# Kernel optimization log

Hardware: AMD Instinct MI355X
Metric: run time of the kernel (lower is better)

The kernel has to match this reference:

```python
import jax, jax.numpy as jnp
import numpy as np

B, S, D, E, F = 2, 1024, 1024, 14, 2048

def setup_inputs() -> dict:
    key = jax.random.key(0)
    k0, k1, k2, k3 = jax.random.split(key, 4)
    h = jax.random.normal(k0, (B, S, D), jnp.float32)
    gate_w = jax.random.normal(k1, (E, D), jnp.float32) * 0.02
    # kaiming-uniform-ish scale for expert weights
    w1 = jax.random.normal(k2, (E, D, F), jnp.float32) * (1.0 / np.sqrt(D).astype(np.float32))
    b1 = jnp.zeros((E, F), jnp.float32)
    w2 = jax.random.normal(k3, (E, F, D), jnp.float32) * (1.0 / np.sqrt(F).astype(np.float32))
    b2 = jnp.zeros((E, D), jnp.float32)
    return {"h": h, "gate_w": gate_w, "w1": w1, "b1": b1, "w2": w2, "b2": b2}

def reference(h, gate_w, w1, b1, w2, b2):
    # Eval-mode forward (no expert dropout, router_step=None, return_aux=False path)
    Bb, Ss, Dd = h.shape
    x = h.reshape(Bb * Ss, Dd)                       # (N, D)
    logits = x @ gate_w.T                            # (N, E)
    probs = jax.nn.softmax(logits, axis=-1)
    top2_p, top2_i = jax.lax.top_k(probs, 2)         # (N, 2)
    w = top2_p / jnp.maximum(top2_p.sum(-1, keepdims=True), 1e-10)
    # dense all-experts FFN
    hh = jnp.einsum('nd,edf->nef', x, w1) + b1       # (N, E, F)
    hh = jax.nn.gelu(hh, approximate=False)          # torch F.gelu default = exact erf
    all_out = jnp.einsum('nef,efd->ned', hh, w2) + b2  # (N, E, D)
    n = jnp.arange(x.shape[0])
    out0 = all_out[n, top2_i[:, 0]]                  # (N, D)
    out1 = all_out[n, top2_i[:, 1]]
    moe_out = w[:, 0:1] * out0 + w[:, 1:2] * out1
    result = jnp.clip(x + moe_out, -100.0, 100.0).reshape(Bb, Ss, Dd)
    return result
```

## Files before the change

kernel.cpp:

```cpp
#include <hip/hip_runtime.h>
#include <cstdint>
#include <cstddef>

#define NTOK 2048
#define DDIM 1024
#define FDIM 2048
#define NEXP 14
#define MAXT 2048

typedef __attribute__((ext_vector_type(8))) short short8;
typedef __attribute__((ext_vector_type(4))) float floatx4;

__device__ __forceinline__ unsigned pack2bf(float lo, float hi) {
    unsigned a = __float_as_uint(lo), b = __float_as_uint(hi);
    return ((a + 0x8000u) >> 16) | ((b + 0x8000u) & 0xffff0000u);
}
__device__ __forceinline__ unsigned short f2bf1(float f) {
    return (unsigned short)((__float_as_uint(f) + 0x8000u) >> 16);
}

__device__ __forceinline__ void glds16(const void* g, void* lds) {
    __builtin_amdgcn_global_load_lds((const __attribute__((address_space(1))) unsigned*)g,
                                     (__attribute__((address_space(3))) unsigned*)lds, 16, 0, 0);
}

__global__ __launch_bounds__(256) void cvtx_kernel(const float* __restrict__ x,
                                                   unsigned short* __restrict__ xb,
                                                   int* __restrict__ cnt) {
    if (blockIdx.x == 0 && threadIdx.x < NEXP) cnt[threadIdx.x] = 0;
    const size_t i = ((size_t)blockIdx.x * 256 + threadIdx.x) * 8;
    float4 a = *(const float4*)(x + i);
    float4 b = *(const float4*)(x + i + 4);
    uint4 u;
    u.x = pack2bf(a.x, a.y); u.y = pack2bf(a.z, a.w);
    u.z = pack2bf(b.x, b.y); u.w = pack2bf(b.z, b.w);
    *(uint4*)(xb + i) = u;
}

__global__ __launch_bounds__(256) void gate_kernel(
    const float* __restrict__ x, const float* __restrict__ gw,
    int* __restrict__ cnt, int* __restrict__ lists, float* __restrict__ wt)
{
    const int wave = threadIdx.x >> 6, lane = threadIdx.x & 63;
    const int n = blockIdx.x * 4 + wave;
    float part[NEXP];
#pragma unroll
    for (int e = 0; e < NEXP; ++e) part[e] = 0.f;
    const float4* xr = (const float4*)(x + (size_t)n * DDIM);
#pragma unroll
    for (int kk = 0; kk < 4; ++kk) {
        const float4 xv = xr[kk * 64 + lane];
#pragma unroll
        for (int e = 0; e < NEXP; ++e) {
            const float4 g = ((const float4*)(gw + e * DDIM))[kk * 64 + lane];
            part[e] = fmaf(xv.x, g.x, fmaf(xv.y, g.y, fmaf(xv.z, g.z, fmaf(xv.w, g.w, part[e]))));
        }
    }
#pragma unroll
    for (int e = 0; e < NEXP; ++e) {
        float v = part[e];
        for (int off = 32; off; off >>= 1) v += __shfl_xor(v, off);
        part[e] = v;
    }
    int i0 = 0; float l0 = part[0];
#pragma unroll
    for (int e = 1; e < NEXP; ++e) if (part[e] > l0) { l0 = part[e]; i0 = e; }
    int i1 = -1; float l1 = -3.0e38f;
#pragma unroll
    for (int e = 0; e < NEXP; ++e) if (e != i0 && part[e] > l1) { l1 = part[e]; i1 = e; }
    if (lane == 0) {
        const float r  = __expf(l1 - l0);
        wt[2 * n]     = 1.f / (1.f + r);
        wt[2 * n + 1] = r / (1.f + r);
        int p0 = atomicAdd(&cnt[i0], 1); lists[i0 * MAXT + p0] = 2 * n;
        int p1 = atomicAdd(&cnt[i1], 1); lists[i1 * MAXT + p1] = 2 * n + 1;
    }
}

#define MAXJOBS 78
__global__ void jobs_kernel(const int* __restrict__ cnt, int* __restrict__ job_e,
                            int* __restrict__ job_mt, int* __restrict__ njobs) {
    if (threadIdx.x == 0) {
        int J = 0;
        for (int e = 0; e < NEXP; ++e) {
            const int m = (cnt[e] + 63) >> 6;
            for (int i = 0; i < m; ++i) { job_e[J] = e; job_mt[J] = i; ++J; }
        }
        njobs[0] = J;
    }
}

__global__ __launch_bounds__(256) void gemm1_kernel(
    const unsigned short* __restrict__ xb, const float* __restrict__ w1,
    const float* __restrict__ b1, const int* __restrict__ cnt,
    const int* __restrict__ lists, const int* __restrict__ job_e,
    const int* __restrict__ job_mt, const int* __restrict__ njobs,
    unsigned short* __restrict__ hh)
{
    const int j = blockIdx.y;
    if (j >= njobs[0]) return;
    const int e = job_e[j], mt = job_mt[j], nt = blockIdx.x;
    const int count = cnt[e];
    const int* list = lists + e * MAXT + mt * 64;
    const int mloc = min(64, count - mt * 64);

    __shared__ __align__(16) unsigned short As[2][64 * 32];
    __shared__ __align__(16) unsigned short Bs[2][128 * 32];

    const int t = threadIdx.x, lane = t & 63, wave = t >> 6;
    const int lrow = lane & 15, lq = lane >> 4;
    const int wn = wave * 32;

    const int arow = wave * 16 + (lane >> 2);
    const int atok = list[min(arow, mloc - 1)] >> 1;
    const unsigned short* aG = xb + (size_t)atok * DDIM + (lane & 3) * 8;
    const int bn = t & 127, bg = t >> 7;
    const float* bG = w1 + (size_t)e * DDIM * FDIM + nt * 128 + bn;

    floatx4 acc[4][2];
#pragma unroll
    for (int i = 0; i < 4; ++i)
#pragma unroll
        for (int jn = 0; jn < 2; ++jn) acc[i][jn] = (floatx4)0.f;

    float br[2][8];
    glds16(aG, &As[0][wave * 512]);
#pragma unroll
    for (int c = 0; c < 2; ++c) {
        const int kc = bg + 2 * c;
#pragma unroll
        for (int jj = 0; jj < 8; ++jj) br[c][jj] = bG[(size_t)(kc * 8 + jj) * FDIM];
    }
#pragma unroll
    for (int c = 0; c < 2; ++c) {
        const int kc = bg + 2 * c;
        uint4 u;
        u.x = pack2bf(br[c][0], br[c][1]); u.y = pack2bf(br[c][2], br[c][3]);
        u.z = pack2bf(br[c][4], br[c][5]); u.w = pack2bf(br[c][6], br[c][7]);
        *(uint4*)&Bs[0][bn * 32 + ((kc ^ (bn & 3)) * 8)] = u;
    }
#pragma unroll
    for (int c = 0; c < 2; ++c) {
        const int kc = bg + 2 * c;
#pragma unroll
        for (int jj = 0; jj < 8; ++jj) br[c][jj] = bG[(size_t)(32 + kc * 8 + jj) * FDIM];
    }

    int p = 0;
    for (int k0 = 0; k0 < DDIM; k0 += 32) {
        __syncthreads();
        if (k0 + 32 < DDIM) {
            glds16(aG + k0 + 32, &As[p ^ 1][wave * 512]);
#pragma unroll
            for (int c = 0; c < 2; ++c) {
                const int kc = bg + 2 * c;
                uint4 u;
                u.x = pack2bf(br[c][0], br[c][1]); u.y = pack2bf(br[c][2], br[c][3]);
                u.z = pack2bf(br[c][4], br[c][5]); u.w = pack2bf(br[c][6], br[c][7]);
                *(uint4*)&Bs[p ^ 1][bn * 32 + ((kc ^ (bn & 3)) * 8)] = u;
            }
        }
        if (k0 + 64 < DDIM) {
#pragma unroll
            for (int c = 0; c < 2; ++c) {
                const int kc = bg + 2 * c;
#pragma unroll
                for (int jj = 0; jj < 8; ++jj) br[c][jj] = bG[(size_t)(k0 + 64 + kc * 8 + jj) * FDIM];
            }
        }
        short8 af[4], bf[2];
#pragma unroll
        for (int i = 0; i < 4; ++i)
            af[i] = *(const short8*)&As[p][(i * 16 + lrow) * 32 + lq * 8];
#pragma unroll
        for (int jn = 0; jn < 2; ++jn) {
            const int n = wn + jn * 16 + lrow;
            bf[jn] = *(const short8*)&Bs[p][n * 32 + ((lq ^ (n & 3)) * 8)];
        }
#pragma unroll
        for (int i = 0; i < 4; ++i)
#pragma unroll
            for (int jn = 0; jn < 2; ++jn)
                acc[i][jn] = __builtin_amdgcn_mfma_f32_16x16x32_bf16(af[i], bf[jn], acc[i][jn], 0, 0, 0);
        p ^= 1;
    }
#pragma unroll
    for (int jn = 0; jn < 2; ++jn) {
        const int n = nt * 128 + wn + jn * 16 + lrow;
        const float bias = b1[e * FDIM + n];
#pragma unroll
        for (int i = 0; i < 4; ++i) {
#pragma unroll
            for (int r = 0; r < 4; ++r) {
                const int m = i * 16 + lq * 4 + r;
                if (m < mloc) {
                    const int pp = list[m];
                    float v = acc[i][jn][r] + bias;
                    v = 0.5f * v * (1.0f + erff(v * 0.70710678118654752f));
                    hh[(size_t)pp * FDIM + n] = f2bf1(v);
                }
            }
        }
    }
}

__global__ __launch_bounds__(256) void gemm2_kernel(
    const unsigned short* __restrict__ hh, const float* __restrict__ w2,
    const float* __restrict__ b2, const int* __restrict__ cnt,
    const int* __restrict__ lists, const int* __restrict__ job_e,
    const int* __restrict__ job_mt, const int* __restrict__ njobs,
    const float* __restrict__ wt, float* __restrict__ out0, float* __restrict__ out1)
{
    const int j = blockIdx.y;
    if (j >= njobs[0]) return;
    const int e = job_e[j], mt = job_mt[j], nt = blockIdx.x;
    const int count = cnt[e];
    const int* list = lists + e * MAXT + mt * 64;
    const int mloc = min(64, count - mt * 64);

    __shared__ __align__(16) unsigned short As[2][64 * 32];
    __shared__ __align__(16) unsigned short Bs[2][64 * 32];

    const int t = threadIdx.x, lane = t & 63, wave = t >> 6;
    const int lrow = lane & 15, lq = lane >> 4;
    const int wm = (wave & 1) * 32, wn = (wave >> 1) * 16;

    const int arow = wave * 16 + (lane >> 2);
    const int apair = list[min(arow, mloc - 1)];
    const unsigned short* aG = hh + (size_t)apair * FDIM + (lane & 3) * 8;
    const int bn = t & 63, bkc = t >> 6;
    const float* bG = w2 + (size_t)e * FDIM * DDIM + nt * 64 + bn;

    floatx4 acc[2][2];
#pragma unroll
    for (int i = 0; i < 2; ++i)
#pragma unroll
        for (int jn = 0; jn < 2; ++jn) acc[i][jn] = (floatx4)0.f;

    float br[8];
    glds16(aG, &As[0][wave * 512]);
#pragma unroll
    for (int jj = 0; jj < 8; ++jj) br[jj] = bG[(size_t)(bkc * 8 + jj) * DDIM];
    {
        uint4 u;
        u.x = pack2bf(br[0], br[1]); u.y = pack2bf(br[2], br[3]);
        u.z = pack2bf(br[4], br[5]); u.w = pack2bf(br[6], br[7]);
        *(uint4*)&Bs[0][bn * 32 + ((bkc ^ (bn & 3)) * 8)] = u;
    }
#pragma unroll
    for (int jj = 0; jj < 8; ++jj) br[jj] = bG[(size_t)(32 + bkc * 8 + jj) * DDIM];

    int p = 0;
    for (int k0 = 0; k0 < FDIM; k0 += 32) {
        __syncthreads();
        if (k0 + 32 < FDIM) {
            glds16(aG + k0 + 32, &As[p ^ 1][wave * 512]);
            uint4 u;
            u.x = pack2bf(br[0], br[1]); u.y = pack2bf(br[2], br[3]);
            u.z = pack2bf(br[4], br[5]); u.w = pack2bf(br[6], br[7]);
            *(uint4*)&Bs[p ^ 1][bn * 32 + ((bkc ^ (bn & 3)) * 8)] = u;
        }
        if (k0 + 64 < FDIM) {
#pragma unroll
            for (int jj = 0; jj < 8; ++jj) br[jj] = bG[(size_t)(k0 + 64 + bkc * 8 + jj) * DDIM];
        }
        short8 af[2], bf[2];
#pragma unroll
        for (int i = 0; i < 2; ++i)
            af[i] = *(const short8*)&As[p][(wm + i * 16 + lrow) * 32 + lq * 8];
#pragma unroll
        for (int jn = 0; jn < 2; ++jn) {
            const int n = wn + jn * 16 + lrow;
            bf[jn] = *(const short8*)&Bs[p][((wn * 2) + jn * 16 + lrow) * 32 + ((lq ^ (((wn * 2) + jn * 16 + lrow) & 3)) * 8)];
        }
#pragma unroll
        for (int i = 0; i < 2; ++i)
#pragma unroll
            for (int jn = 0; jn < 2; ++jn)
                acc[i][jn] = __builtin_amdgcn_mfma_f32_16x16x32_bf16(af[i], bf[jn], acc[i][jn], 0, 0, 0);
        p ^= 1;
    }
#pragma unroll
    for (int jn = 0; jn < 2; ++jn) {
        const int n = nt * 64 + (wn * 2) + jn * 16 + lrow;
        const float bias = b2[e * DDIM + n];
#pragma unroll
        for (int i = 0; i < 2; ++i) {
#pragma unroll
            for (int r = 0; r < 4; ++r) {
                const int m = wm + i * 16 + lq * 4 + r;
                if (m < mloc) {
                    const int pp = list[m];
                    const int tok = pp >> 1;
                    const float v = (acc[i][jn][r] + bias) * wt[pp];
                    float* dst = (pp & 1) ? out1 : out0;
                    dst[(size_t)tok * DDIM + n] = v;
                }
            }
        }
    }
}

__global__ __launch_bounds__(256) void finalize_kernel(
    const float* __restrict__ x, const float* __restrict__ o1,
    float* __restrict__ out)
{
    const size_t i = ((size_t)blockIdx.x * 256 + threadIdx.x) * 4;
    float4 xv = *(const float4*)(x + i);
    float4 a  = *(const float4*)(out + i);
    float4 b  = *(const float4*)(o1 + i);
    float4 r;
    r.x = fminf(fmaxf(xv.x + a.x + b.x, -100.f), 100.f);
    r.y = fminf(fmaxf(xv.y + a.y + b.y, -100.f), 100.f);
    r.z = fminf(fmaxf(xv.z + a.z + b.z, -100.f), 100.f);
    r.w = fminf(fmaxf(xv.w + a.w + b.w, -100.f), 100.f);
    *(float4*)(out + i) = r;
}

extern "C" void kernel_launch(void* const* d_in, const int* in_sizes, int n_in,
                              void* d_out, int out_size, void* d_ws, size_t ws_size,
                              hipStream_t stream) {
    const float* h  = (const float*)d_in[0];
    const float* gw = (const float*)d_in[1];
    const float* w1 = (const float*)d_in[2];
    const float* b1 = (const float*)d_in[3];
    const float* w2 = (const float*)d_in[4];
    const float* b2 = (const float*)d_in[5];
    float* out = (float*)d_out;

    char* ws = (char*)d_ws;
    int*   cnt    = (int*)ws;
    int*   lists  = (int*)(ws + 256);
    float* wt     = (float*)(ws + 114944);
    int*   job_e  = (int*)(ws + 131328);
    int*   job_mt = (int*)(ws + 131840);
    int*   njobs  = (int*)(ws + 132352);
    unsigned short* xb = (unsigned short*)(ws + 262144);
    float* o1     = (float*)(ws + 262144 + 4194304);
    unsigned short* hhb = (unsigned short*)(ws + 262144 + 4194304 + 8388608);

    cvtx_kernel<<<NTOK * DDIM / (256 * 8), 256, 0, stream>>>(h, xb, cnt);
    gate_kernel<<<NTOK / 4, 256, 0, stream>>>(h, gw, cnt, lists, wt);
    jobs_kernel<<<1, 64, 0, stream>>>(cnt, job_e, job_mt, njobs);
    gemm1_kernel<<<dim3(FDIM / 128, MAXJOBS), 256, 0, stream>>>(xb, w1, b1, cnt, lists, job_e, job_mt, njobs, hhb);
    gemm2_kernel<<<dim3(DDIM / 64, MAXJOBS), 256, 0, stream>>>(hhb, w2, b2, cnt, lists, job_e, job_mt, njobs, wt, out, o1);
    finalize_kernel<<<NTOK * DDIM / (256 * 4), 256, 0, stream>>>(h, o1, out);
}
```

Measured before the change: 433.7 us.

## Pre-convert expert weights to transposed bf16 and stream via direct LDS loads

Result: slower. 541.9 us (+25.0%).

```diff
diff --git a/kernel.cpp b/kernel.cpp
--- a/kernel.cpp
+++ b/kernel.cpp
@@ -37,6 +37,28 @@
     *(uint4*)(xb + i) = u;
 }
 
+__global__ __launch_bounds__(256) void cvtw_kernel(
+    const float* __restrict__ src, unsigned short* __restrict__ dst,
+    int K, int N, int kt, int tpe)
+{
+    const int b = blockIdx.x;
+    const int e = b / tpe, r = b % tpe;
+    const int n = (r / kt) * 64 + (threadIdx.x & 63);
+    const int kq = (r % kt) * 128 + (threadIdx.x >> 6) * 32;
+    const float* s = src + (size_t)e * K * N + (size_t)kq * N + n;
+    float v[32];
+#pragma unroll
+    for (int j = 0; j < 32; ++j) v[j] = s[(size_t)j * N];
+    unsigned us[16];
+#pragma unroll
+    for (int q = 0; q < 16; ++q) us[q] = pack2bf(v[2 * q], v[2 * q + 1]);
+    unsigned short* d = dst + (size_t)e * K * N + (size_t)n * K + kq;
+    *(uint4*)(d)      = uint4{us[0],  us[1],  us[2],  us[3]};
+    *(uint4*)(d + 8)  = uint4{us[4],  us[5],  us[6],  us[7]};
+    *(uint4*)(d + 16) = uint4{us[8],  us[9],  us[10], us[11]};
+    *(uint4*)(d + 24) = uint4{us[12], us[13], us[14], us[15]};
+}
+
 __global__ __launch_bounds__(256) void gate_kernel(
     const float* __restrict__ x, const float* __restrict__ gw,
     int* __restrict__ cnt, int* __restrict__ lists, float* __restrict__ wt)
@@ -91,7 +113,7 @@
 }
 
 __global__ __launch_bounds__(256) void gemm1_kernel(
-    const unsigned short* __restrict__ xb, const float* __restrict__ w1,
+    const unsigned short* __restrict__ xb, const unsigned short* __restrict__ w1t,
     const float* __restrict__ b1, const int* __restrict__ cnt,
     const int* __restrict__ lists, const int* __restrict__ job_e,
     const int* __restrict__ job_mt, const int* __restrict__ njobs,
@@ -107,15 +129,15 @@
     __shared__ __align__(16) unsigned short As[2][64 * 32];
     __shared__ __align__(16) unsigned short Bs[2][128 * 32];
 
-    const int t = threadIdx.x, lane = t & 63, wave = t >> 6;
+    const int t = threadIdx.x, lane = t & 63, w = t >> 6;
     const int lrow = lane & 15, lq = lane >> 4;
-    const int wn = wave * 32;
-
-    const int arow = wave * 16 + (lane >> 2);
+
+    const int arow = w * 16 + lrow;
     const int atok = list[min(arow, mloc - 1)] >> 1;
-    const unsigned short* aG = xb + (size_t)atok * DDIM + (lane & 3) * 8;
-    const int bn = t & 127, bg = t >> 7;
-    const float* bG = w1 + (size_t)e * DDIM * FDIM + nt * 128 + bn;
+    const unsigned short* aG = xb + (size_t)atok * DDIM + lq * 8;
+    const int nA = nt * 128 + w * 16 + lrow;
+    const unsigned short* bG0 = w1t + ((size_t)e * FDIM + nA) * DDIM + lq * 8;
+    const unsigned short* bG1 = bG0 + (size_t)64 * DDIM;
 
     floatx4 acc[4][2];
 #pragma unroll
@@ -123,60 +145,25 @@
 #pragma unroll
         for (int jn = 0; jn < 2; ++jn) acc[i][jn] = (floatx4)0.f;
 
-    float br[2][8];
-    glds16(aG, &As[0][wave * 512]);
-#pragma unroll
-    for (int c = 0; c < 2; ++c) {
-        const int kc = bg + 2 * c;
-#pragma unroll
-        for (int jj = 0; jj < 8; ++jj) br[c][jj] = bG[(size_t)(kc * 8 + jj) * FDIM];
-    }
-#pragma unroll
-    for (int c = 0; c < 2; ++c) {
-        const int kc = bg + 2 * c;
-        uint4 u;
-        u.x = pack2bf(br[c][0], br[c][1]); u.y = pack2bf(br[c][2], br[c][3]);
-        u.z = pack2bf(br[c][4], br[c][5]); u.w = pack2bf(br[c][6], br[c][7]);
-        *(uint4*)&Bs[0][bn * 32 + ((kc ^ (bn & 3)) * 8)] = u;
-    }
-#pragma unroll
-    for (int c = 0; c < 2; ++c) {
-        const int kc = bg + 2 * c;
-#pragma unroll
-        for (int jj = 0; jj < 8; ++jj) br[c][jj] = bG[(size_t)(32 + kc * 8 + jj) * FDIM];
-    }
+    glds16(aG, &As[0][w * 512]);
+    glds16(bG0, &Bs[0][w * 512]);
+    glds16(bG1, &Bs[0][(w + 4) * 512]);
 
     int p = 0;
     for (int k0 = 0; k0 < DDIM; k0 += 32) {
         __syncthreads();
         if (k0 + 32 < DDIM) {
-            glds16(aG + k0 + 32, &As[p ^ 1][wave * 512]);
-#pragma unroll
-            for (int c = 0; c < 2; ++c) {
-                const int kc = bg + 2 * c;
-                uint4 u;
-                u.x = pack2bf(br[c][0], br[c][1]); u.y = pack2bf(br[c][2], br[c][3]);
-                u.z = pack2bf(br[c][4], br[c][5]); u.w = pack2bf(br[c][6], br[c][7]);
-                *(uint4*)&Bs[p ^ 1][bn * 32 + ((kc ^ (bn & 3)) * 8)] = u;
-            }
-        }
-        if (k0 + 64 < DDIM) {
-#pragma unroll
-            for (int c = 0; c < 2; ++c) {
-                const int kc = bg + 2 * c;
-#pragma unroll
-                for (int jj = 0; jj < 8; ++jj) br[c][jj] = bG[(size_t)(k0 + 64 + kc * 8 + jj) * FDIM];
-            }
+            glds16(aG + k0 + 32, &As[p ^ 1][w * 512]);
+            glds16(bG0 + k0 + 32, &Bs[p ^ 1][w * 512]);
+            glds16(bG1 + k0 + 32, &Bs[p ^ 1][(w + 4) * 512]);
         }
         short8 af[4], bf[2];
 #pragma unroll
         for (int i = 0; i < 4; ++i)
-            af[i] = *(const short8*)&As[p][(i * 16 + lrow) * 32 + lq * 8];
-#pragma unroll
-        for (int jn = 0; jn < 2; ++jn) {
-            const int n = wn + jn * 16 + lrow;
-            bf[jn] = *(const short8*)&Bs[p][n * 32 + ((lq ^ (n & 3)) * 8)];
-        }
+            af[i] = *(const short8*)&As[p][i * 512 + lane * 8];
+#pragma unroll
+        for (int jn = 0; jn < 2; ++jn)
+            bf[jn] = *(const short8*)&Bs[p][(2 * w + jn) * 512 + lane * 8];
 #pragma unroll
         for (int i = 0; i < 4; ++i)
 #pragma unroll
@@ -186,7 +173,7 @@
     }
 #pragma unroll
     for (int jn = 0; jn < 2; ++jn) {
-        const int n = nt * 128 + wn + jn * 16 + lrow;
+        const int n = nt * 128 + w * 32 + jn * 16 + lrow;
         const float bias = b1[e * FDIM + n];
 #pragma unroll
         for (int i = 0; i < 4; ++i) {
@@ -205,7 +192,7 @@
 }
 
 __global__ __launch_bounds__(256) void gemm2_kernel(
-    const unsigned short* __restrict__ hh, const float* __restrict__ w2,
+    const unsigned short* __restrict__ hh, const unsigned short* __restrict__ w2t,
     const float* __restrict__ b2, const int* __restrict__ cnt,
     const int* __restrict__ lists, const int* __restrict__ job_e,
     const int* __restrict__ job_mt, const int* __restrict__ njobs,
@@ -218,18 +205,18 @@
     const int* list = lists + e * MAXT + mt * 64;
     const int mloc = min(64, count - mt * 64);
 
-    __shared__ __align__(16) unsigned short As[2][64 * 32];
-    __shared__ __align__(16) unsigned short Bs[2][64 * 32];
-
-    const int t = threadIdx.x, lane = t & 63, wave = t >> 6;
+    __shared__ __align__(16) unsigned short As[2][64 * 64];
+    __shared__ __align__(16) unsigned short Bs[2][64 * 64];
+
+    const int t = threadIdx.x, lane = t & 63, w = t >> 6;
     const int lrow = lane & 15, lq = lane >> 4;
-    const int wm = (wave & 1) * 32, wn = (wave >> 1) * 16;
-
-    const int arow = wave * 16 + (lane >> 2);
+    const int wm = (w & 1) * 32, wn = (w >> 1) * 32;
+
+    const int arow = w * 16 + lrow;
     const int apair = list[min(arow, mloc - 1)];
-    const unsigned short* aG = hh + (size_t)apair * FDIM + (lane & 3) * 8;
-    const int bn = t & 63, bkc = t >> 6;
-    const float* bG = w2 + (size_t)e * FDIM * DDIM + nt * 64 + bn;
+    const unsigned short* aG = hh + (size_t)apair * FDIM + lq * 8;
+    const int nB = nt * 64 + w * 16 + lrow;
+    const unsigned short* bG = w2t + ((size_t)e * DDIM + nB) * FDIM + lq * 8;
 
     floatx4 acc[2][2];
 #pragma unroll
@@ -237,52 +224,40 @@
 #pragma unroll
         for (int jn = 0; jn < 2; ++jn) acc[i][jn] = (floatx4)0.f;
 
-    float br[8];
-    glds16(aG, &As[0][wave * 512]);
-#pragma unroll
-    for (int jj = 0; jj < 8; ++jj) br[jj] = bG[(size_t)(bkc * 8 + jj) * DDIM];
-    {
-        uint4 u;
-        u.x = pack2bf(br[0], br[1]); u.y = pack2bf(br[2], br[3]);
-        u.z = pack2bf(br[4], br[5]); u.w = pack2bf(br[6], br[7]);
-        *(uint4*)&Bs[0][bn * 32 + ((bkc ^ (bn & 3)) * 8)] = u;
-    }
-#pragma unroll
-    for (int jj = 0; jj < 8; ++jj) br[jj] = bG[(size_t)(32 + bkc * 8 + jj) * DDIM];
+    glds16(aG,      &As[0][w * 1024]);
+    glds16(aG + 32, &As[0][w * 1024 + 512]);
+    glds16(bG,      &Bs[0][w * 1024]);
+    glds16(bG + 32, &Bs[0][w * 1024 + 512]);
 
     int p = 0;
-    for (int k0 = 0; k0 < FDIM; k0 += 32) {
+    for (int k0 = 0; k0 < FDIM; k0 += 64) {
         __syncthreads();
-        if (k0 + 32 < FDIM) {
-            glds16(aG + k0 + 32, &As[p ^ 1][wave * 512]);
-            uint4 u;
-            u.x = pack2bf(br[0], br[1]); u.y = pack2bf(br[2], br[3]);
-            u.z = pack2bf(br[4], br[5]); u.w = pack2bf(br[6], br[7]);
-            *(uint4*)&Bs[p ^ 1][bn * 32 + ((bkc ^ (bn & 3)) * 8)] = u;
-        }
         if (k0 + 64 < FDIM) {
-#pragma unroll
-            for (int jj = 0; jj < 8; ++jj) br[jj] = bG[(size_t)(k0 + 64 + bkc * 8 + jj) * DDIM];
-        }
-        short8 af[2], bf[2];
-#pragma unroll
-        for (int i = 0; i < 2; ++i)
-            af[i] = *(const short8*)&As[p][(wm + i * 16 + lrow) * 32 + lq * 8];
-#pragma unroll
-        for (int jn = 0; jn < 2; ++jn) {
-            const int n = wn + jn * 16 + lrow;
-            bf[jn] = *(const short8*)&Bs[p][((wn * 2) + jn * 16 + lrow) * 32 + ((lq ^ (((wn * 2) + jn * 16 + lrow) & 3)) * 8)];
-        }
-#pragma unroll
-        for (int i = 0; i < 2; ++i)
+            glds16(aG + k0 + 64, &As[p ^ 1][w * 1024]);
+            glds16(aG + k0 + 96, &As[p ^ 1][w * 1024 + 512]);
+            glds16(bG + k0 + 64, &Bs[p ^ 1][w * 1024]);
+            glds16(bG + k0 + 96, &Bs[p ^ 1][w * 1024 + 512]);
+        }
+#pragma unroll
+        for (int s = 0; s < 2; ++s) {
+            short8 af[2], bf[2];
+#pragma unroll
+            for (int i = 0; i < 2; ++i)
+                af[i] = *(const short8*)&As[p][((w & 1) * 2 + i) * 1024 + s * 512 + lane * 8];
 #pragma unroll
             for (int jn = 0; jn < 2; ++jn)
-                acc[i][jn] = __builtin_amdgcn_mfma_f32_16x16x32_bf16(af[i], bf[jn], acc[i][jn], 0, 0, 0);
+                bf[jn] = *(const short8*)&Bs[p][((w >> 1) * 2 + jn) * 1024 + s * 512 + lane * 8];
+#pragma unroll
+            for (int i = 0; i < 2; ++i)
+#pragma unroll
+                for (int jn = 0; jn < 2; ++jn)
+                    acc[i][jn] = __builtin_amdgcn_mfma_f32_16x16x32_bf16(af[i], bf[jn], acc[i][jn], 0, 0, 0);
+        }
         p ^= 1;
     }
 #pragma unroll
     for (int jn = 0; jn < 2; ++jn) {
-        const int n = nt * 64 + (wn * 2) + jn * 16 + lrow;
+        const int n = nt * 64 + wn + jn * 16 + lrow;
         const float bias = b2[e * DDIM + n];
 #pragma unroll
         for (int i = 0; i < 2; ++i) {
@@ -335,14 +310,17 @@
     int*   job_e  = (int*)(ws + 131328);
     int*   job_mt = (int*)(ws + 131840);
     int*   njobs  = (int*)(ws + 132352);
-    unsigned short* xb = (unsigned short*)(ws + 262144);
+    unsigned short* xb  = (unsigned short*)(ws + 262144);
     float* o1     = (float*)(ws + 262144 + 4194304);
     unsigned short* hhb = (unsigned short*)(ws + 262144 + 4194304 + 8388608);
+    unsigned short* wtb = (unsigned short*)(ws + 262144 + 4194304 + 8388608 + 16777216);
 
     cvtx_kernel<<<NTOK * DDIM / (256 * 8), 256, 0, stream>>>(h, xb, cnt);
     gate_kernel<<<NTOK / 4, 256, 0, stream>>>(h, gw, cnt, lists, wt);
     jobs_kernel<<<1, 64, 0, stream>>>(cnt, job_e, job_mt, njobs);
-    gemm1_kernel<<<dim3(FDIM / 128, MAXJOBS), 256, 0, stream>>>(xb, w1, b1, cnt, lists, job_e, job_mt, njobs, hhb);
-    gemm2_kernel<<<dim3(DDIM / 64, MAXJOBS), 256, 0, stream>>>(hhb, w2, b2, cnt, lists, job_e, job_mt, njobs, wt, out, o1);
+    cvtw_kernel<<<NEXP * 256, 256, 0, stream>>>(w1, wtb, DDIM, FDIM, DDIM / 128, 256);
+    gemm1_kernel<<<dim3(FDIM / 128, MAXJOBS), 256, 0, stream>>>(xb, wtb, b1, cnt, lists, job_e, job_mt, njobs, hhb);
+    cvtw_kernel<<<NEXP * 256, 256, 0, stream>>>(w2, wtb, FDIM, DDIM, FDIM / 128, 256);
+    gemm2_kernel<<<dim3(DDIM / 64, MAXJOBS), 256, 0, stream>>>(hhb, wtb, b2, cnt, lists, job_e, job_mt, njobs, wt, out, o1);
     finalize_kernel<<<NTOK * DDIM / (256 * 4), 256, 0, stream>>>(h, o1, out);
 }
```
